# Kernel tuning notes

Hardware: AMD Instinct MI355X
Metric: run time of the kernel (lower is better)

## Reference

```python
import jax, jax.numpy as jnp
import numpy as np

DIM = 256
HEADS = 8
DIM_HEAD = 64
INNER = HEADS * DIM_HEAD
NUM_BANDS = 16          # hard-coded in __init__
MAX_FREQ = 16.0         # hard-coded in __init__
NORM_SCALE = 51.0       # hard-coded in __init__
RPE_DIM = (NUM_BANDS * 2 + 1) * 2  # 66


def fourier_encode(x, max_freq, num_bands):
    # x: [...] -> [..., 2*num_bands+1]  (sin bands, cos bands, raw)
    x = x[..., None]
    scales = jnp.linspace(1.0, max_freq / 2.0, num_bands, dtype=x.dtype)
    xs = x * scales * jnp.pi
    return jnp.concatenate([jnp.sin(xs), jnp.cos(xs), x], axis=-1)


def rpe_features(query_pos, key_pos):
    # delta[b,i,j] = key_pos[b,j] - query_pos[b,i]  -> [B,Nq,Nk,2]
    delta = key_pos[:, None, :, :] - query_pos[:, :, None, :]
    dx = delta[..., 0] / NORM_SCALE
    dy = delta[..., 1] / NORM_SCALE
    dx = dx / (1.0 + jnp.abs(dx))
    dy = dy / (1.0 + jnp.abs(dy))
    x_enc = fourier_encode(dx, MAX_FREQ, NUM_BANDS)
    y_enc = fourier_encode(dy, MAX_FREQ, NUM_BANDS)
    return jnp.concatenate([x_enc, y_enc], axis=-1)  # [B,Nq,Nk,RPE_DIM]


def setup_inputs() -> dict:
    key = jax.random.key(0)
    ks = jax.random.split(key, 8)
    B, N = 1, 512
    x = jax.random.normal(ks[0], (B, N, DIM), dtype=jnp.float32)
    positions = jax.random.uniform(ks[1], (B, N, 2), dtype=jnp.float32) * 512.0
    s = 0.02
    Wq = jax.random.normal(ks[2], (DIM, INNER), dtype=jnp.float32) * s
    Wk = jax.random.normal(ks[3], (DIM + RPE_DIM, INNER), dtype=jnp.float32) * s
    Wv = jax.random.normal(ks[4], (DIM, INNER), dtype=jnp.float32) * s
    Wo = jax.random.normal(ks[5], (INNER, DIM), dtype=jnp.float32) * s
    bo = jnp.zeros((DIM,), dtype=jnp.float32)
    return {"x": x, "positions": positions, "Wq": Wq, "Wk": Wk, "Wv": Wv, "Wo": Wo, "bo": bo}


def reference(x, positions, Wq, Wk, Wv, Wo, bo):
    B, N, D = x.shape
    H, d = HEADS, DIM_HEAD
    scale = d ** -0.5

    rpe = rpe_features(positions, positions)          # [B,N,N,R]
    q = (x @ Wq).reshape(B, N, H, d)                  # [B,N,H,d]
    v = (x @ Wv).reshape(B, N, H, d)

    # k_ij = W_k @ concat(x_j, rpe_ij); split Wk to avoid expanding x to [B,N,N,D]
    Wk_x, Wk_r = Wk[:D], Wk[D:]
    k_content = x @ Wk_x                               # [B,N,INNER] (key j part)
    k_rpe = jnp.einsum('bijr,re->bije', rpe, Wk_r)     # [B,N,N,INNER]
    k = (k_content[:, None, :, :] + k_rpe).reshape(B, N, N, H, d)

    scores = jnp.einsum('bihd,bijhd->bhij', q, k) * scale
    attn = jax.nn.softmax(scores, axis=-1)
    out = jnp.einsum('bhij,bjhd->bihd', attn, v).reshape(B, N, H * d)
    return out @ Wo + bo
```

## Files before the change

### kernel.cpp

```cpp
#include <hip/hip_runtime.h>
#include <math.h>

#define NQ      512
#define DMODEL  256
#define DINNER  512
#define NH      8
#define DHEAD   64
#define SCALE   0.125f
#define PI_F    3.14159265358979323846f

#define Q_OFF   0
#define KC_OFF  262144
#define V_OFF   524288
#define QW_OFF  786432
#define IN_OFF  1064960

__global__ __launch_bounds__(256) void k_proj(
    const float* __restrict__ x, const float* __restrict__ Wq,
    const float* __restrict__ Wk, const float* __restrict__ Wv,
    float* __restrict__ ws)
{
    const int z = blockIdx.z;
    const float* W = (z == 0) ? Wq : (z == 1) ? Wk : Wv;
    float* out = ws + ((z == 0) ? Q_OFF : (z == 1) ? KC_OFF : V_OFF);

    __shared__ alignas(16) float Xs[32][68];
    __shared__ alignas(16) float Bs[32][64];

    const int tx = threadIdx.x, ty = threadIdx.y;
    const int tid = ty * 16 + tx;
    const int row0 = blockIdx.y * 64, col0 = blockIdx.x * 64;

    float acc[4][4] = {};

    for (int k0 = 0; k0 < DMODEL; k0 += 32) {
        {
            const int m = tid >> 2;
            const int kk0 = (tid & 3) * 8;
            const float* src = x + (row0 + m) * DMODEL + k0 + kk0;
            float4 a0 = *(const float4*)(src);
            float4 a1 = *(const float4*)(src + 4);
            Xs[kk0 + 0][m] = a0.x; Xs[kk0 + 1][m] = a0.y;
            Xs[kk0 + 2][m] = a0.z; Xs[kk0 + 3][m] = a0.w;
            Xs[kk0 + 4][m] = a1.x; Xs[kk0 + 5][m] = a1.y;
            Xs[kk0 + 6][m] = a1.z; Xs[kk0 + 7][m] = a1.w;
        }
        {
            const int kk = tid >> 3;
            const int n0 = (tid & 7) * 8;
            const float* src = W + (k0 + kk) * DINNER + col0 + n0;
            *(float4*)&Bs[kk][n0]     = *(const float4*)(src);
            *(float4*)&Bs[kk][n0 + 4] = *(const float4*)(src + 4);
        }
        __syncthreads();
        #pragma unroll
        for (int kk = 0; kk < 32; ++kk) {
            float4 a4 = *(const float4*)&Xs[kk][ty * 4];
            float4 b4 = *(const float4*)&Bs[kk][tx * 4];
            float a[4] = {a4.x, a4.y, a4.z, a4.w};
            float b[4] = {b4.x, b4.y, b4.z, b4.w};
            #pragma unroll
            for (int ia = 0; ia < 4; ++ia)
                #pragma unroll
                for (int ib = 0; ib < 4; ++ib)
                    acc[ia][ib] += a[ia] * b[ib];
        }
        __syncthreads();
    }
    #pragma unroll
    for (int ia = 0; ia < 4; ++ia) {
        float4 o = make_float4(acc[ia][0], acc[ia][1], acc[ia][2], acc[ia][3]);
        *(float4*)&out[(row0 + ty * 4 + ia) * DINNER + col0 + tx * 4] = o;
    }
}

__global__ __launch_bounds__(256) void k_qw(
    const float* __restrict__ Wk, float* __restrict__ ws)
{
    const float* q = ws + Q_OFF;
    float* qW = ws + QW_OFF;
    const int h  = blockIdx.x >> 4;
    const int i0 = (blockIdx.x & 15) * 32;

    __shared__ float WrT[64][67];
    __shared__ alignas(16) float Qs[32][68];
    const int tid = threadIdx.x;

    for (int idx = tid; idx < 66 * 64; idx += 256) {
        int r = idx >> 6, d = idx & 63;
        WrT[d][r] = Wk[(DMODEL + r) * DINNER + h * DHEAD + d];
    }
    for (int idx = tid; idx < 32 * 16; idx += 256) {
        int m = idx >> 4, dq = (idx & 15) * 4;
        *(float4*)&Qs[m][dq] = *(const float4*)&q[(i0 + m) * DINNER + h * DHEAD + dq];
    }
    __syncthreads();

    for (int idx = tid; idx < 32 * 66; idx += 256) {
        int m = idx / 66, r = idx - m * 66;
        float acc = 0.f;
        #pragma unroll
        for (int d0 = 0; d0 < 64; d0 += 4) {
            float4 qf = *(const float4*)&Qs[m][d0];
            acc += qf.x * WrT[d0 + 0][r] + qf.y * WrT[d0 + 1][r]
                 + qf.z * WrT[d0 + 2][r] + qf.w * WrT[d0 + 3][r];
        }
        int p = (r < 32) ? r : (r == 32) ? 64 : (r < 65) ? (r - 1) : 65;
        qW[(i0 + m) * 544 + h * 68 + p] = acc * SCALE;
    }
}

__device__ __forceinline__ float rpe_eval(float2 pq, float2 pk, const float4* cw)
{
    float dxr = (pk.x - pq.x) * (1.0f / 51.0f);
    float dyr = (pk.y - pq.y) * (1.0f / 51.0f);
    float dx = dxr / (1.0f + fabsf(dxr));
    float dy = dyr / (1.0f + fabsf(dyr));
    float thx = dx * PI_F, dlx = dx * (PI_F * 7.0f / 15.0f);
    float thy = dy * PI_F, dly = dy * (PI_F * 7.0f / 15.0f);
    float sxa, cxa, sxb, cxb, sya, cya, syb, cyb;
    __sincosf(thx, &sxa, &cxa);
    __sincosf(thx + dlx, &sxb, &cxb);
    __sincosf(thy, &sya, &cya);
    __sincosf(thy + dly, &syb, &cyb);
    const float Kx = 2.0f * __cosf(dlx);
    const float Ky = 2.0f * __cosf(dly);
    float acc = 0.f;
    #pragma unroll
    for (int g = 0; g < 4; ++g) {
        float4 wsx = cw[g], wcx = cw[4 + g], wsy = cw[8 + g], wcy = cw[12 + g];
        #pragma unroll
        for (int k = 0; k < 4; ++k) {
            float a = (&wsx.x)[k], b = (&wcx.x)[k], c = (&wsy.x)[k], e = (&wcy.x)[k];
            acc += sxa * a + cxa * b + sya * c + cya * e;
            float t;
            t = Kx * sxb - sxa; sxa = sxb; sxb = t;
            t = Kx * cxb - cxa; cxa = cxb; cxb = t;
            t = Ky * syb - sya; sya = syb; syb = t;
            t = Ky * cyb - cya; cya = cyb; cyb = t;
        }
    }
    float4 tw = cw[16];
    acc += dx * tw.x + dy * tw.y;
    return acc;
}

__device__ __forceinline__ float wave_max(float v)
{
    #pragma unroll
    for (int off = 32; off; off >>= 1) v = fmaxf(v, __shfl_xor(v, off));
    return v;
}
__device__ __forceinline__ float wave_sum(float v)
{
    #pragma unroll
    for (int off = 32; off; off >>= 1) v += __shfl_xor(v, off);
    return v;
}

__global__ __launch_bounds__(256) void k_attn(
    const float* __restrict__ pos, float* __restrict__ ws)
{
    const float* q  = ws + Q_OFF;
    const float* kc = ws + KC_OFF;
    const float* v  = ws + V_OFF;
    const float* qW = ws + QW_OFF;
    float* inner    = ws + IN_OFF;

    const int h  = blockIdx.x >> 6;
    const int i0 = (blockIdx.x & 63) * 8;
    const int tid = threadIdx.x;
    const int w = tid >> 6, l = tid & 63;
    const int iw = w * 2;

    __shared__ alignas(16) float Qs[64][12];
    __shared__ alignas(16) float qWs[8][68];
    __shared__ float2 posQs[8];
    __shared__ alignas(16) float Ks[64][68];
    __shared__ alignas(16) float Vs[64][68];
    __shared__ float2 posKs[64];
    __shared__ alignas(16) float Ps[8][68];

    if (tid < 128) {
        int m = tid >> 4, d4 = (tid & 15) * 4;
        float4 qv = *(const float4*)&q[(i0 + m) * DINNER + h * DHEAD + d4];
        Qs[d4 + 0][m] = qv.x; Qs[d4 + 1][m] = qv.y;
        Qs[d4 + 2][m] = qv.z; Qs[d4 + 3][m] = qv.w;
    }
    for (int idx = tid; idx < 8 * 68; idx += 256) {
        int m = idx / 68, c = idx - m * 68;
        qWs[m][c] = qW[(i0 + m) * 544 + h * 68 + c];
    }
    if (tid < 8) posQs[tid] = *(const float2*)&pos[(i0 + tid) * 2];

    float m0 = -1e30f, m1 = -1e30f;
    float ls0 = 0.f, ls1 = 0.f;
    float acc0 = 0.f, acc1 = 0.f;

    const float4* cw0 = (const float4*)&qWs[iw][0];
    const float4* cw1 = (const float4*)&qWs[iw + 1][0];

    for (int jt = 0; jt < 8; ++jt) {
        const int j0 = jt * 64;
        __syncthreads();
        {
            const int jj = tid >> 2, dg = (tid & 3) * 16;
            const float* sk = kc + (j0 + jj) * DINNER + h * DHEAD + dg;
            float4 a = *(const float4*)(sk),     b = *(const float4*)(sk + 4),
                   c = *(const float4*)(sk + 8), d = *(const float4*)(sk + 12);
            Ks[dg +  0][jj] = a.x; Ks[dg +  1][jj] = a.y; Ks[dg +  2][jj] = a.z; Ks[dg +  3][jj] = a.w;
            Ks[dg +  4][jj] = b.x; Ks[dg +  5][jj] = b.y; Ks[dg +  6][jj] = b.z; Ks[dg +  7][jj] = b.w;
            Ks[dg +  8][jj] = c.x; Ks[dg +  9][jj] = c.y; Ks[dg + 10][jj] = c.z; Ks[dg + 11][jj] = c.w;
            Ks[dg + 12][jj] = d.x; Ks[dg + 13][jj] = d.y; Ks[dg + 14][jj] = d.z; Ks[dg + 15][jj] = d.w;
            const float* sv = v + (j0 + jj) * DINNER + h * DHEAD + dg;
            *(float4*)&Vs[jj][dg +  0] = *(const float4*)(sv);
            *(float4*)&Vs[jj][dg +  4] = *(const float4*)(sv + 4);
            *(float4*)&Vs[jj][dg +  8] = *(const float4*)(sv + 8);
            *(float4*)&Vs[jj][dg + 12] = *(const float4*)(sv + 12);
            if (tid < 64) posKs[tid] = *(const float2*)&pos[(j0 + tid) * 2];
        }
        __syncthreads();

        float s0 = 0.f, s1 = 0.f;
        #pragma unroll 8
        for (int d = 0; d < 64; ++d) {
            float kf = Ks[d][l];
            float2 q2 = *(const float2*)&Qs[d][iw];
            s0 += q2.x * kf;
            s1 += q2.y * kf;
        }
        s0 *= SCALE; s1 *= SCALE;

        float2 pk = posKs[l];
        s0 += rpe_eval(posQs[iw],     pk, cw0);
        s1 += rpe_eval(posQs[iw + 1], pk, cw1);

        {
            float mt = wave_max(s0);
            float mn = fmaxf(m0, mt);
            float rs = __expf(m0 - mn);
            float p  = __expf(s0 - mn);
            ls0 = ls0 * rs + wave_sum(p);
            acc0 *= rs;
            m0 = mn;
            Ps[iw][l] = p;
        }
        {
            float mt = wave_max(s1);
            float mn = fmaxf(m1, mt);
            float rs = __expf(m1 - mn);
            float p  = __expf(s1 - mn);
            ls1 = ls1 * rs + wave_sum(p);
            acc1 *= rs;
            m1 = mn;
            Ps[iw + 1][l] = p;
        }
        __syncthreads();

        #pragma unroll
        for (int jg = 0; jg < 16; ++jg) {
            float4 p0 = *(const float4*)&Ps[iw][jg * 4];
            float4 p1 = *(const float4*)&Ps[iw + 1][jg * 4];
            float v0 = Vs[jg * 4 + 0][l];
            float v1 = Vs[jg * 4 + 1][l];
            float v2 = Vs[jg * 4 + 2][l];
            float v3 = Vs[jg * 4 + 3][l];
            acc0 += p0.x * v0 + p0.y * v1 + p0.z * v2 + p0.w * v3;
            acc1 += p1.x * v0 + p1.y * v1 + p1.z * v2 + p1.w * v3;
        }
    }

    inner[(i0 + iw)     * DINNER + h * DHEAD + l] = acc0 / ls0;
    inner[(i0 + iw + 1) * DINNER + h * DHEAD + l] = acc1 / ls1;
}

__global__ __launch_bounds__(256) void k_out(
    const float* __restrict__ Wo, const float* __restrict__ bo,
    float* __restrict__ ws, float* __restrict__ outp)
{
    const float* inner = ws + IN_OFF;
    const int c0 = blockIdx.x * 32;
    const int i0 = blockIdx.y * 32;

    __shared__ alignas(16) float Xs[32][36];
    __shared__ alignas(16) float Bs[32][32];
    const int tx = threadIdx.x, ty = threadIdx.y;
    const int tid = ty * 16 + tx;

    float acc[2][2] = {};
    for (int k0 = 0; k0 < DINNER; k0 += 32) {
        {
            const int m = tid >> 3;
            const int kk0 = (tid & 7) * 4;
            float4 a4 = *(const float4*)&inner[(i0 + m) * DINNER + k0 + kk0];
            Xs[kk0 + 0][m] = a4.x; Xs[kk0 + 1][m] = a4.y;
            Xs[kk0 + 2][m] = a4.z; Xs[kk0 + 3][m] = a4.w;
        }
        {
            const int kk = tid >> 3;
            const int n0 = (tid & 7) * 4;
            *(float4*)&Bs[kk][n0] = *(const float4*)&Wo[(k0 + kk) * DMODEL + c0 + n0];
        }
        __syncthreads();
        #pragma unroll
        for (int kk = 0; kk < 32; ++kk) {
            float2 a2 = *(const float2*)&Xs[kk][ty * 2];
            float2 b2 = *(const float2*)&Bs[kk][tx * 2];
            acc[0][0] += a2.x * b2.x;
            acc[0][1] += a2.x * b2.y;
            acc[1][0] += a2.y * b2.x;
            acc[1][1] += a2.y * b2.y;
        }
        __syncthreads();
    }
    #pragma unroll
    for (int ia = 0; ia < 2; ++ia) {
        float2 o;
        o.x = acc[ia][0] + bo[c0 + tx * 2 + 0];
        o.y = acc[ia][1] + bo[c0 + tx * 2 + 1];
        *(float2*)&outp[(i0 + ty * 2 + ia) * DMODEL + c0 + tx * 2] = o;
    }
}

extern "C" void kernel_launch(void* const* d_in, const int* in_sizes, int n_in,
                              void* d_out, int out_size, void* d_ws, size_t ws_size,
                              hipStream_t stream)
{
    const float* x   = (const float*)d_in[0];
    const float* pos = (const float*)d_in[1];
    const float* Wq  = (const float*)d_in[2];
    const float* Wk  = (const float*)d_in[3];
    const float* Wv  = (const float*)d_in[4];
    const float* Wo  = (const float*)d_in[5];
    const float* bo  = (const float*)d_in[6];
    float* out = (float*)d_out;
    float* ws  = (float*)d_ws;

    k_proj<<<dim3(8, 8, 3), dim3(16, 16), 0, stream>>>(x, Wq, Wk, Wv, ws);
    k_qw<<<dim3(128), dim3(256), 0, stream>>>(Wk, ws);
    k_attn<<<dim3(512), dim3(256), 0, stream>>>(pos, ws);
    k_out<<<dim3(8, 16), dim3(16, 16), 0, stream>>>(Wo, bo, ws, out);
}
```

Baseline: 155.6 us.

## Split attention over key chunks with per-thread query rows and merge kernel

Restructures attention into a split-K (flash-decoding style) scheme. Each block handles 64 queries against one 64-key chunk for one head, with each thread owning a query row whose q and RPE weights are kept in registers. Partial max, sum and accumulators are combined across waves in LDS, written to workspace, and reduced by a new merge kernel. This removes the per-tile wave shuffles and barriers of the old online softmax and raises per-thread work, at the cost of an extra launch, heavy register pressure and extra global traffic for the partials.

```diff
diff --git a/kernel.cpp b/kernel.cpp
--- a/kernel.cpp
+++ b/kernel.cpp
@@ -14,6 +14,9 @@
 #define V_OFF   524288
 #define QW_OFF  786432
 #define IN_OFF  1064960
+#define PA_OFF  1327104
+#define PM_OFF  3424256
+#define PL_OFF  3457024
 
 __global__ __launch_bounds__(256) void k_proj(
     const float* __restrict__ x, const float* __restrict__ Wq,
@@ -110,168 +113,201 @@
     }
 }
 
-__device__ __forceinline__ float rpe_eval(float2 pq, float2 pk, const float4* cw)
-{
-    float dxr = (pk.x - pq.x) * (1.0f / 51.0f);
-    float dyr = (pk.y - pq.y) * (1.0f / 51.0f);
-    float dx = dxr / (1.0f + fabsf(dxr));
-    float dy = dyr / (1.0f + fabsf(dyr));
-    float thx = dx * PI_F, dlx = dx * (PI_F * 7.0f / 15.0f);
-    float thy = dy * PI_F, dly = dy * (PI_F * 7.0f / 15.0f);
-    float sxa, cxa, sxb, cxb, sya, cya, syb, cyb;
-    __sincosf(thx, &sxa, &cxa);
-    __sincosf(thx + dlx, &sxb, &cxb);
-    __sincosf(thy, &sya, &cya);
-    __sincosf(thy + dly, &syb, &cyb);
-    const float Kx = 2.0f * __cosf(dlx);
-    const float Ky = 2.0f * __cosf(dly);
-    float acc = 0.f;
-    #pragma unroll
-    for (int g = 0; g < 4; ++g) {
-        float4 wsx = cw[g], wcx = cw[4 + g], wsy = cw[8 + g], wcy = cw[12 + g];
-        #pragma unroll
-        for (int k = 0; k < 4; ++k) {
-            float a = (&wsx.x)[k], b = (&wcx.x)[k], c = (&wsy.x)[k], e = (&wcy.x)[k];
-            acc += sxa * a + cxa * b + sya * c + cya * e;
-            float t;
-            t = Kx * sxb - sxa; sxa = sxb; sxb = t;
-            t = Kx * cxb - cxa; cxa = cxb; cxb = t;
-            t = Ky * syb - sya; sya = syb; syb = t;
-            t = Ky * cyb - cya; cya = cyb; cyb = t;
-        }
-    }
-    float4 tw = cw[16];
-    acc += dx * tw.x + dy * tw.y;
-    return acc;
-}
-
-__device__ __forceinline__ float wave_max(float v)
-{
-    #pragma unroll
-    for (int off = 32; off; off >>= 1) v = fmaxf(v, __shfl_xor(v, off));
-    return v;
-}
-__device__ __forceinline__ float wave_sum(float v)
-{
-    #pragma unroll
-    for (int off = 32; off; off >>= 1) v += __shfl_xor(v, off);
-    return v;
-}
-
-__global__ __launch_bounds__(256) void k_attn(
+__global__ __launch_bounds__(256, 2) void k_attn(
     const float* __restrict__ pos, float* __restrict__ ws)
 {
     const float* q  = ws + Q_OFF;
     const float* kc = ws + KC_OFF;
     const float* v  = ws + V_OFF;
     const float* qW = ws + QW_OFF;
-    float* inner    = ws + IN_OFF;
-
-    const int h  = blockIdx.x >> 6;
-    const int i0 = (blockIdx.x & 63) * 8;
+    float* pacc = ws + PA_OFF;
+    float* pm   = ws + PM_OFF;
+    float* pl   = ws + PL_OFF;
+
+    const int c  = blockIdx.x;
+    const int it = blockIdx.y;
+    const int h  = blockIdx.z;
     const int tid = threadIdx.x;
     const int w = tid >> 6, l = tid & 63;
-    const int iw = w * 2;
-
-    __shared__ alignas(16) float Qs[64][12];
-    __shared__ alignas(16) float qWs[8][68];
-    __shared__ float2 posQs[8];
+    const int i = it * 64 + l;
+    const int j0 = c * 64;
+
     __shared__ alignas(16) float Ks[64][68];
     __shared__ alignas(16) float Vs[64][68];
     __shared__ float2 posKs[64];
-    __shared__ alignas(16) float Ps[8][68];
-
-    if (tid < 128) {
-        int m = tid >> 4, d4 = (tid & 15) * 4;
-        float4 qv = *(const float4*)&q[(i0 + m) * DINNER + h * DHEAD + d4];
-        Qs[d4 + 0][m] = qv.x; Qs[d4 + 1][m] = qv.y;
-        Qs[d4 + 2][m] = qv.z; Qs[d4 + 3][m] = qv.w;
-    }
-    for (int idx = tid; idx < 8 * 68; idx += 256) {
-        int m = idx / 68, c = idx - m * 68;
-        qWs[m][c] = qW[(i0 + m) * 544 + h * 68 + c];
-    }
-    if (tid < 8) posQs[tid] = *(const float2*)&pos[(i0 + tid) * 2];
-
-    float m0 = -1e30f, m1 = -1e30f;
-    float ls0 = 0.f, ls1 = 0.f;
-    float acc0 = 0.f, acc1 = 0.f;
-
-    const float4* cw0 = (const float4*)&qWs[iw][0];
-    const float4* cw1 = (const float4*)&qWs[iw + 1][0];
-
-    for (int jt = 0; jt < 8; ++jt) {
-        const int j0 = jt * 64;
-        __syncthreads();
-        {
-            const int jj = tid >> 2, dg = (tid & 3) * 16;
-            const float* sk = kc + (j0 + jj) * DINNER + h * DHEAD + dg;
-            float4 a = *(const float4*)(sk),     b = *(const float4*)(sk + 4),
-                   c = *(const float4*)(sk + 8), d = *(const float4*)(sk + 12);
-            Ks[dg +  0][jj] = a.x; Ks[dg +  1][jj] = a.y; Ks[dg +  2][jj] = a.z; Ks[dg +  3][jj] = a.w;
-            Ks[dg +  4][jj] = b.x; Ks[dg +  5][jj] = b.y; Ks[dg +  6][jj] = b.z; Ks[dg +  7][jj] = b.w;
-            Ks[dg +  8][jj] = c.x; Ks[dg +  9][jj] = c.y; Ks[dg + 10][jj] = c.z; Ks[dg + 11][jj] = c.w;
-            Ks[dg + 12][jj] = d.x; Ks[dg + 13][jj] = d.y; Ks[dg + 14][jj] = d.z; Ks[dg + 15][jj] = d.w;
-            const float* sv = v + (j0 + jj) * DINNER + h * DHEAD + dg;
-            *(float4*)&Vs[jj][dg +  0] = *(const float4*)(sv);
-            *(float4*)&Vs[jj][dg +  4] = *(const float4*)(sv + 4);
-            *(float4*)&Vs[jj][dg +  8] = *(const float4*)(sv + 8);
-            *(float4*)&Vs[jj][dg + 12] = *(const float4*)(sv + 12);
-            if (tid < 64) posKs[tid] = *(const float2*)&pos[(j0 + tid) * 2];
-        }
-        __syncthreads();
-
-        float s0 = 0.f, s1 = 0.f;
-        #pragma unroll 8
-        for (int d = 0; d < 64; ++d) {
-            float kf = Ks[d][l];
-            float2 q2 = *(const float2*)&Qs[d][iw];
-            s0 += q2.x * kf;
-            s1 += q2.y * kf;
-        }
-        s0 *= SCALE; s1 *= SCALE;
-
-        float2 pk = posKs[l];
-        s0 += rpe_eval(posQs[iw],     pk, cw0);
-        s1 += rpe_eval(posQs[iw + 1], pk, cw1);
-
-        {
-            float mt = wave_max(s0);
-            float mn = fmaxf(m0, mt);
-            float rs = __expf(m0 - mn);
-            float p  = __expf(s0 - mn);
-            ls0 = ls0 * rs + wave_sum(p);
-            acc0 *= rs;
-            m0 = mn;
-            Ps[iw][l] = p;
-        }
-        {
-            float mt = wave_max(s1);
-            float mn = fmaxf(m1, mt);
-            float rs = __expf(m1 - mn);
-            float p  = __expf(s1 - mn);
-            ls1 = ls1 * rs + wave_sum(p);
-            acc1 *= rs;
-            m1 = mn;
-            Ps[iw + 1][l] = p;
-        }
-        __syncthreads();
-
-        #pragma unroll
-        for (int jg = 0; jg < 16; ++jg) {
-            float4 p0 = *(const float4*)&Ps[iw][jg * 4];
-            float4 p1 = *(const float4*)&Ps[iw + 1][jg * 4];
-            float v0 = Vs[jg * 4 + 0][l];
-            float v1 = Vs[jg * 4 + 1][l];
-            float v2 = Vs[jg * 4 + 2][l];
-            float v3 = Vs[jg * 4 + 3][l];
-            acc0 += p0.x * v0 + p0.y * v1 + p0.z * v2 + p0.w * v3;
-            acc1 += p1.x * v0 + p1.y * v1 + p1.z * v2 + p1.w * v3;
-        }
-    }
-
-    inner[(i0 + iw)     * DINNER + h * DHEAD + l] = acc0 / ls0;
-    inner[(i0 + iw + 1) * DINNER + h * DHEAD + l] = acc1 / ls1;
+    __shared__ float pmL[4][64];
+    __shared__ float plL[4][64];
+
+    {
+        const int jj = tid >> 2, dg = (tid & 3) * 16;
+        const float* sk = kc + (j0 + jj) * DINNER + h * DHEAD + dg;
+        *(float4*)&Ks[jj][dg +  0] = *(const float4*)(sk);
+        *(float4*)&Ks[jj][dg +  4] = *(const float4*)(sk + 4);
+        *(float4*)&Ks[jj][dg +  8] = *(const float4*)(sk + 8);
+        *(float4*)&Ks[jj][dg + 12] = *(const float4*)(sk + 12);
+        const float* sv = v + (j0 + jj) * DINNER + h * DHEAD + dg;
+        *(float4*)&Vs[jj][dg +  0] = *(const float4*)(sv);
+        *(float4*)&Vs[jj][dg +  4] = *(const float4*)(sv + 4);
+        *(float4*)&Vs[jj][dg +  8] = *(const float4*)(sv + 8);
+        *(float4*)&Vs[jj][dg + 12] = *(const float4*)(sv + 12);
+        if (tid < 64) posKs[tid] = *(const float2*)&pos[(j0 + tid) * 2];
+    }
+
+    float4 qv[16];
+    const float* qrow = q + i * DINNER + h * DHEAD;
+    #pragma unroll
+    for (int d4 = 0; d4 < 16; ++d4) qv[d4] = *(const float4*)(qrow + d4 * 4);
+    float4 cw[17];
+    const float* qwrow = qW + i * 544 + h * 68;
+    #pragma unroll
+    for (int p4 = 0; p4 < 17; ++p4) cw[p4] = *(const float4*)(qwrow + p4 * 4);
+    const float2 pq = *(const float2*)&pos[i * 2];
+
+    __syncthreads();
+
+    const int jb = w * 16;
+    float sreg[16];
+    float M = -1e30f;
+
+    #pragma unroll
+    for (int t = 0; t < 16; ++t) {
+        const int jr = jb + t;
+        float s0 = 0.f, s1 = 0.f, s2 = 0.f, s3 = 0.f;
+        #pragma unroll
+        for (int d4 = 0; d4 < 16; ++d4) {
+            float4 kv = *(const float4*)&Ks[jr][d4 * 4];
+            s0 += qv[d4].x * kv.x; s1 += qv[d4].y * kv.y;
+            s2 += qv[d4].z * kv.z; s3 += qv[d4].w * kv.w;
+        }
+        float s = (s0 + s1) + (s2 + s3);
+
+        float2 pk = posKs[jr];
+        float dxr = (pk.x - pq.x) * (1.0f / 51.0f);
+        float dyr = (pk.y - pq.y) * (1.0f / 51.0f);
+        float dx = __fdividef(dxr, 1.0f + fabsf(dxr));
+        float dy = __fdividef(dyr, 1.0f + fabsf(dyr));
+        float thx = dx * PI_F, dlx = dx * (PI_F * 7.0f / 15.0f);
+        float thy = dy * PI_F, dly = dy * (PI_F * 7.0f / 15.0f);
+        float sxa, cxa, sxb, cxb, sya, cya, syb, cyb;
+        __sincosf(thx,       &sxa, &cxa);
+        __sincosf(thx + dlx, &sxb, &cxb);
+        __sincosf(thy,       &sya, &cya);
+        __sincosf(thy + dly, &syb, &cyb);
+        float Kx = 2.0f * (cxa * cxb + sxa * sxb);
+        float Ky = 2.0f * (cya * cyb + sya * syb);
+        float r0 = 0.f, r1 = 0.f, r2 = 0.f, r3 = 0.f;
+        #pragma unroll
+        for (int g = 0; g < 4; ++g) {
+            float4 wsx = cw[g], wcx = cw[4 + g], wsy = cw[8 + g], wcy = cw[12 + g];
+            #pragma unroll
+            for (int k = 0; k < 4; ++k) {
+                r0 += sxa * (&wsx.x)[k];
+                r1 += cxa * (&wcx.x)[k];
+                r2 += sya * (&wsy.x)[k];
+                r3 += cya * (&wcy.x)[k];
+                float tt;
+                tt = Kx * sxb - sxa; sxa = sxb; sxb = tt;
+                tt = Kx * cxb - cxa; cxa = cxb; cxb = tt;
+                tt = Ky * syb - sya; sya = syb; syb = tt;
+                tt = Ky * cyb - cya; cya = cyb; cyb = tt;
+            }
+        }
+        float rpe = (r0 + r1) + (r2 + r3) + dx * cw[16].x + dy * cw[16].y;
+        float score = s * SCALE + rpe;
+        sreg[t] = score;
+        M = fmaxf(M, score);
+    }
+
+    float4 av[16];
+    #pragma unroll
+    for (int d4 = 0; d4 < 16; ++d4) av[d4] = make_float4(0.f, 0.f, 0.f, 0.f);
+    float lsum = 0.f;
+    #pragma unroll
+    for (int t = 0; t < 16; ++t) {
+        float p = __expf(sreg[t] - M);
+        lsum += p;
+        const int jr = jb + t;
+        #pragma unroll
+        for (int d4 = 0; d4 < 16; ++d4) {
+            float4 vv = *(const float4*)&Vs[jr][d4 * 4];
+            av[d4].x += p * vv.x; av[d4].y += p * vv.y;
+            av[d4].z += p * vv.z; av[d4].w += p * vv.w;
+        }
+    }
+
+    pmL[w][l] = M; plL[w][l] = lsum;
+    __syncthreads();
+    float m0 = pmL[0][l], m1 = pmL[1][l], m2 = pmL[2][l], m3 = pmL[3][l];
+    float Mg = fmaxf(fmaxf(m0, m1), fmaxf(m2, m3));
+    float e = __expf(M - Mg);
+    #pragma unroll
+    for (int d4 = 0; d4 < 16; ++d4) {
+        av[d4].x *= e; av[d4].y *= e; av[d4].z *= e; av[d4].w *= e;
+    }
+    float (*Sacc)[68] = Ks;
+    if (w == 0) {
+        #pragma unroll
+        for (int d4 = 0; d4 < 16; ++d4) *(float4*)&Sacc[l][d4 * 4] = av[d4];
+    }
+    __syncthreads();
+    if (w == 1) {
+        #pragma unroll
+        for (int d4 = 0; d4 < 16; ++d4) {
+            float4 sv = *(const float4*)&Sacc[l][d4 * 4];
+            sv.x += av[d4].x; sv.y += av[d4].y; sv.z += av[d4].z; sv.w += av[d4].w;
+            *(float4*)&Sacc[l][d4 * 4] = sv;
+        }
+    }
+    __syncthreads();
+    if (w == 2) {
+        #pragma unroll
+        for (int d4 = 0; d4 < 16; ++d4) {
+            float4 sv = *(const float4*)&Sacc[l][d4 * 4];
+            sv.x += av[d4].x; sv.y += av[d4].y; sv.z += av[d4].z; sv.w += av[d4].w;
+            *(float4*)&Sacc[l][d4 * 4] = sv;
+        }
+    }
+    __syncthreads();
+    if (w == 3) {
+        float Lg = plL[0][l] * __expf(m0 - Mg) + plL[1][l] * __expf(m1 - Mg)
+                 + plL[2][l] * __expf(m2 - Mg) + plL[3][l] * __expf(m3 - Mg);
+        float* prow = pacc + ((size_t)((h * NQ + i) * 8 + c)) * 64;
+        #pragma unroll
+        for (int d4 = 0; d4 < 16; ++d4) {
+            float4 sv = *(const float4*)&Sacc[l][d4 * 4];
+            sv.x += av[d4].x; sv.y += av[d4].y; sv.z += av[d4].z; sv.w += av[d4].w;
+            *(float4*)&prow[d4 * 4] = sv;
+        }
+        pm[(h * NQ + i) * 8 + c] = Mg;
+        pl[(h * NQ + i) * 8 + c] = Lg;
+    }
+}
+
+__global__ __launch_bounds__(256) void k_merge(float* __restrict__ ws)
+{
+    float* inner      = ws + IN_OFF;
+    const float* pacc = ws + PA_OFF;
+    const float* pm   = ws + PM_OFF;
+    const float* pl   = ws + PL_OFF;
+
+    const int g = blockIdx.x * 4 + (threadIdx.x >> 6);
+    const int l = threadIdx.x & 63;
+
+    float mv[8];
+    #pragma unroll
+    for (int cc = 0; cc < 8; ++cc) mv[cc] = pm[g * 8 + cc];
+    float Mg = mv[0];
+    #pragma unroll
+    for (int cc = 1; cc < 8; ++cc) Mg = fmaxf(Mg, mv[cc]);
+    float L = 0.f, a = 0.f;
+    #pragma unroll
+    for (int cc = 0; cc < 8; ++cc) {
+        float e = __expf(mv[cc] - Mg);
+        L += pl[g * 8 + cc] * e;
+        a += pacc[(size_t)(g * 8 + cc) * 64 + l] * e;
+    }
+    const int h = g >> 9, i = g & 511;
+    inner[i * DINNER + h * DHEAD + l] = a / L;
 }
 
 __global__ __launch_bounds__(256) void k_out(
@@ -338,6 +374,7 @@
 
     k_proj<<<dim3(8, 8, 3), dim3(16, 16), 0, stream>>>(x, Wq, Wk, Wv, ws);
     k_qw<<<dim3(128), dim3(256), 0, stream>>>(Wk, ws);
-    k_attn<<<dim3(512), dim3(256), 0, stream>>>(pos, ws);
+    k_attn<<<dim3(8, 8, 8), dim3(256), 0, stream>>>(pos, ws);
+    k_merge<<<dim3(1024), dim3(256), 0, stream>>>(ws);
     k_out<<<dim3(8, 16), dim3(16, 16), 0, stream>>>(Wo, bo, ws, out);
 }
```

Result: faster. 146.7 us (-5.7%).
